# Optimization experiments

Hardware: AMD Instinct MI355X
Metric: run time of the kernel (lower is better)

## Reference

```python
import jax, jax.numpy as jnp
import numpy as np

DIM = 1024

def setup_inputs() -> dict:
    key = jax.random.key(0)
    k1, k2, k3, k4 = jax.random.split(key, 4)
    x = jax.random.normal(k1, (8, 2048, DIM), dtype=jnp.float32)
    # torch Linear weights: y = x @ W.T
    w_qkv = jax.random.normal(k2, (3 * DIM, DIM), dtype=jnp.float32) * (DIM ** -0.5)
    w_proj = jax.random.normal(k3, (DIM, DIM), dtype=jnp.float32) * (DIM ** -0.5)
    b_proj = jax.random.normal(k4, (DIM,), dtype=jnp.float32) * 0.01
    return {"x": x, "w_qkv": w_qkv, "w_proj": w_proj, "b_proj": b_proj}

def reference(x, w_qkv, w_proj, b_proj):
    B, N, C = x.shape
    scale = C ** -0.5
    qkv = jnp.einsum('bnc,dc->bnd', x, w_qkv).reshape(B, N, 3, C)
    q, k, v = qkv[:, :, 0], qkv[:, :, 1], qkv[:, :, 2]  # each [B,N,C]
    attn = jnp.einsum('bnc,bmc->bnm', q, k) * scale      # [B,N,N]
    attn = jax.nn.softmax(attn, axis=-1)
    o = jnp.einsum('bnm,bmc->bnc', attn, v)              # [B,N,C]
    # faithful to torch: (attn@v).transpose(1,2).reshape(B,N,C) permutes data
    o = jnp.swapaxes(o, 1, 2).reshape(B, N, C)
    return jnp.einsum('bnc,dc->bnd', o, w_proj) + b_proj
```

## Files before the change

kernel.cpp:

```cpp
#include <hip/hip_runtime.h>

typedef __bf16 bf16x8_t __attribute__((ext_vector_type(8)));
typedef float f32x4_t __attribute__((ext_vector_type(4)));

#define AS1 __attribute__((address_space(1)))
#define AS3 __attribute__((address_space(3)))

__device__ __forceinline__ unsigned short f2b(float f) {
    unsigned u = __builtin_bit_cast(unsigned, f);
    u += 0x7fffu + ((u >> 16) & 1u);
    return (unsigned short)(u >> 16);
}
__device__ __forceinline__ float b2f(unsigned short s) {
    return __builtin_bit_cast(float, (unsigned)s << 16);
}

__global__ __launch_bounds__(256) void k_f2b(const float* __restrict__ in,
                                             unsigned short* __restrict__ out,
                                             int n4) {
    int i = blockIdx.x * 256 + threadIdx.x;
    if (i >= n4) return;
    float4 v = reinterpret_cast<const float4*>(in)[i];
    ushort4 o;
    o.x = f2b(v.x); o.y = f2b(v.y); o.z = f2b(v.z); o.w = f2b(v.w);
    reinterpret_cast<ushort4*>(out)[i] = o;
}

#define STAGE3(tt, bb) do {                                                    \
    char* dst_ = smem + (bb) * 24576;                                          \
    const size_t kof_ = (size_t)(tt) * 32;                                     \
    __builtin_amdgcn_global_load_lds((const AS1 void*)(pA0 + kof_),            \
        (AS3 void*)(dst_ + wave * 1024), 16, 0, 0);                            \
    __builtin_amdgcn_global_load_lds((const AS1 void*)(pA1 + kof_),            \
        (AS3 void*)(dst_ + 8192 + wave * 1024), 16, 0, 0);                     \
    __builtin_amdgcn_global_load_lds((const AS1 void*)(pB0 + kof_),            \
        (AS3 void*)(dst_ + 16384 + wave * 1024), 16, 0, 0);                    \
} while (0)

__device__ __forceinline__ void gemm_ml_128(
    const unsigned short* __restrict__ A, int lda,
    const unsigned short* __restrict__ B, int ldb,
    int K, char* smem, f32x4_t acc[4][4]) {
    const int tid = threadIdx.x;
    const int wave = tid >> 6, lane = tid & 63;
    const int wm = wave >> 1, wn = wave & 1;
    const int fr = lane & 15, g = lane >> 4;

    const int scolB = ((lane & 3) * 16) ^ (((lane >> 3) & 3) << 4);
    const unsigned short* pA0 = A + (size_t)(wave * 16 + (lane >> 2)) * lda + (scolB >> 1);
    const unsigned short* pA1 = pA0 + (size_t)128 * lda;
    const unsigned short* pB0 = B + (size_t)(wave * 16 + (lane >> 2)) * ldb + (scolB >> 1);

    const int rswz = (g * 16) ^ (((fr >> 1) & 3) << 4);
    int offA[4], offB[4];
#pragma unroll
    for (int mi = 0; mi < 4; ++mi)
        offA[mi] = (wm * 64 + mi * 16 + fr) * 64 + rswz;
#pragma unroll
    for (int ni = 0; ni < 4; ++ni)
        offB[ni] = 16384 + (wn * 64 + ni * 16 + fr) * 64 + rswz;

#pragma unroll
    for (int mi = 0; mi < 4; ++mi)
#pragma unroll
        for (int ni = 0; ni < 4; ++ni)
            acc[mi][ni] = (f32x4_t){0.f, 0.f, 0.f, 0.f};

    const int NT = K >> 5;

    STAGE3(0, 0);
    STAGE3(1, 1);

    int cb = 0;
    for (int t = 0; t < NT; ++t) {
        if (t + 1 < NT) asm volatile("s_waitcnt vmcnt(3)" ::: "memory");
        else            asm volatile("s_waitcnt vmcnt(0)" ::: "memory");
        asm volatile("s_barrier" ::: "memory");
        if (t + 2 < NT) {
            int sb = cb + 2; if (sb >= 3) sb -= 3;
            STAGE3(t + 2, sb);
        }
        const char* rb = smem + cb * 24576;
        bf16x8_t af[4], bfv[4];
#pragma unroll
        for (int mi = 0; mi < 4; ++mi)
            af[mi] = *reinterpret_cast<const bf16x8_t*>(rb + offA[mi]);
#pragma unroll
        for (int ni = 0; ni < 4; ++ni)
            bfv[ni] = *reinterpret_cast<const bf16x8_t*>(rb + offB[ni]);
        __builtin_amdgcn_s_setprio(1);
#pragma unroll
        for (int mi = 0; mi < 4; ++mi)
#pragma unroll
            for (int ni = 0; ni < 4; ++ni)
                acc[mi][ni] = __builtin_amdgcn_mfma_f32_16x16x32_bf16(
                    af[mi], bfv[ni], acc[mi][ni], 0, 0, 0);
        __builtin_amdgcn_s_setprio(0);
        cb = (cb + 1 == 3) ? 0 : cb + 1;
    }
}

#define E128_IDX                                                \
    const int lane = threadIdx.x & 63, wave = threadIdx.x >> 6; \
    const int e_r0 = (wave >> 1) * 64 + (lane >> 4) * 4;        \
    const int e_c0 = (wave & 1) * 64 + (lane & 15);

#define E128_LOOP(...)                                          \
    _Pragma("unroll") for (int mi = 0; mi < 4; ++mi)            \
    _Pragma("unroll") for (int ni = 0; ni < 4; ++ni)            \
    _Pragma("unroll") for (int j = 0; j < 4; ++j) { __VA_ARGS__ }

#define STA(h, i)                                                              \
    __builtin_amdgcn_global_load_lds(                                         \
        (const AS1 void*)(pA + kof + (size_t)((h) * 128 + (i) * 8) * lda),    \
        (AS3 void*)(wb + (h) * 16384 + wave * 2048 + (i) * 1024), 16, 0, 0)
#define STB(h, i)                                                              \
    __builtin_amdgcn_global_load_lds(                                         \
        (const AS1 void*)(pB + kof + (size_t)((h) * 128 + (i) * 8) * ldb),    \
        (AS3 void*)(wb + 32768 + (h) * 16384 + wave * 2048 + (i) * 1024), 16, 0, 0)

#define READ_A(qm)                                                             \
    _Pragma("unroll") for (int mi = 0; mi < 4; ++mi)                           \
        _Pragma("unroll") for (int ks = 0; ks < 2; ++ks)                       \
            af[mi][ks] = *reinterpret_cast<const bf16x8_t*>(rb + offA[qm][mi][ks]);
#define READ_B(qn)                                                             \
    _Pragma("unroll") for (int ni = 0; ni < 2; ++ni)                           \
        _Pragma("unroll") for (int ks = 0; ks < 2; ++ks)                       \
            bf[qn][ni][ks] = *reinterpret_cast<const bf16x8_t*>(rb + offB[qn][ni][ks]);

#define MFMA_QUAD(qm, qn)                                                      \
    __builtin_amdgcn_s_setprio(1);                                             \
    _Pragma("unroll") for (int mi = 0; mi < 4; ++mi)                           \
        _Pragma("unroll") for (int ni = 0; ni < 2; ++ni) {                     \
            acc[qm][qn][mi][ni] = __builtin_amdgcn_mfma_f32_16x16x32_bf16(     \
                af[mi][0], bf[qn][ni][0], acc[qm][qn][mi][ni], 0, 0, 0);       \
            acc[qm][qn][mi][ni] = __builtin_amdgcn_mfma_f32_16x16x32_bf16(     \
                af[mi][1], bf[qn][ni][1], acc[qm][qn][mi][ni], 0, 0, 0);       \
        }                                                                      \
    __builtin_amdgcn_s_setprio(0);

template <bool LAST>
__device__ __forceinline__ void tile_step(
    const char* rb, char* wb, size_t kof,
    const unsigned short* pA, const unsigned short* pB, int lda, int ldb,
    int wave, const int offA[2][4][2], const int offB[2][2][2],
    f32x4_t acc[2][2][4][2]) {
    bf16x8_t af[4][2], bf[2][2][2];
    asm volatile("s_waitcnt vmcnt(2)" ::: "memory");
    asm volatile("s_barrier" ::: "memory");
    if constexpr (!LAST) { STA(0, 0); STA(0, 1); STB(0, 0); STB(0, 1); }
    READ_A(0); READ_B(0); READ_B(1);
    MFMA_QUAD(0, 0);
    MFMA_QUAD(0, 1);
    if constexpr (LAST) asm volatile("s_waitcnt vmcnt(0)" ::: "memory");
    else                asm volatile("s_waitcnt vmcnt(4)" ::: "memory");
    asm volatile("s_barrier" ::: "memory");
    if constexpr (!LAST) { STB(1, 0); STB(1, 1); STA(1, 0); STA(1, 1); }
    READ_A(1);
    MFMA_QUAD(1, 1);
    MFMA_QUAD(1, 0);
}

__device__ __forceinline__ void gemm_ml_256(
    const unsigned short* __restrict__ A, int lda,
    const unsigned short* __restrict__ B, int ldb,
    int K, char* smem, f32x4_t acc[2][2][4][2]) {
    const int tid = threadIdx.x;
    const int wave = tid >> 6, lane = tid & 63;
    const int wsm = (wave >> 2) & 1, wsn = wave & 3;
    const int fr = lane & 15, g = lane >> 4;
    const int srow8 = lane >> 3;
    const int scolB = ((lane & 7) * 16) ^ (srow8 << 4);

    const unsigned short* pA = A + (size_t)(wave * 16 + srow8) * lda + (scolB >> 1);
    const unsigned short* pB = B + (size_t)(wave * 16 + srow8) * ldb + (scolB >> 1);

    int offA[2][4][2], offB[2][2][2];
#pragma unroll
    for (int qm = 0; qm < 2; ++qm)
#pragma unroll
        for (int mi = 0; mi < 4; ++mi)
#pragma unroll
            for (int ks = 0; ks < 2; ++ks)
                offA[qm][mi][ks] = qm * 16384 + (wsm * 64 + mi * 16 + fr) * 128 +
                                   ((ks * 64 + g * 16) ^ ((fr & 7) << 4));
#pragma unroll
    for (int qn = 0; qn < 2; ++qn)
#pragma unroll
        for (int ni = 0; ni < 2; ++ni)
#pragma unroll
            for (int ks = 0; ks < 2; ++ks)
                offB[qn][ni][ks] = 32768 + qn * 16384 + (wsn * 32 + ni * 16 + fr) * 128 +
                                   ((ks * 64 + g * 16) ^ ((fr & 7) << 4));

#pragma unroll
    for (int qm = 0; qm < 2; ++qm)
#pragma unroll
        for (int qn = 0; qn < 2; ++qn)
#pragma unroll
            for (int mi = 0; mi < 4; ++mi)
#pragma unroll
                for (int ni = 0; ni < 2; ++ni)
                    acc[qm][qn][mi][ni] = (f32x4_t){0.f, 0.f, 0.f, 0.f};

    const int NT = K >> 6;

    {
        char* wb = smem;
        const size_t kof = 0;
        STA(0, 0); STA(0, 1);
        STB(0, 0); STB(0, 1);
        STB(1, 0); STB(1, 1);
        STA(1, 0); STA(1, 1);
    }

    for (int t = 0; t < NT - 1; ++t) {
        const char* rb = smem + (size_t)(t & 1) * 65536;
        char* wb = smem + (size_t)((t & 1) ^ 1) * 65536;
        tile_step<false>(rb, wb, (size_t)(t + 1) * 64, pA, pB, lda, ldb,
                         wave, offA, offB, acc);
    }
    {
        const char* rb = smem + (size_t)((NT - 1) & 1) * 65536;
        tile_step<true>(rb, smem, 0, pA, pB, lda, ldb, wave, offA, offB, acc);
    }
}

#define E256_IDX                                                \
    const int lane = threadIdx.x & 63, wave = threadIdx.x >> 6; \
    const int e_r0 = ((wave >> 2) & 1) * 64 + (lane >> 4) * 4;  \
    const int e_c0 = (wave & 3) * 32 + (lane & 15);

#define E256_LOOP(...)                                          \
    _Pragma("unroll") for (int qm = 0; qm < 2; ++qm)            \
    _Pragma("unroll") for (int qn = 0; qn < 2; ++qn)            \
    _Pragma("unroll") for (int mi = 0; mi < 4; ++mi)            \
    _Pragma("unroll") for (int ni = 0; ni < 2; ++ni)            \
    _Pragma("unroll") for (int j = 0; j < 4; ++j) { __VA_ARGS__ }


__global__ __launch_bounds__(512, 4) void k_gemm_qkv_qk(
    const unsigned short* __restrict__ x, const unsigned short* __restrict__ w,
    unsigned short* __restrict__ qk) {
    __shared__ __align__(16) char smem[73728];
    const size_t tm = (size_t)blockIdx.x * 256, tn = (size_t)blockIdx.y * 128;
    f32x4_t acc[4][4];
    gemm_ml_128(x + tm * 1024, 1024, w + tn * 1024, 1024, 1024, smem, acc);
    E128_IDX
    E128_LOOP(
        size_t m = tm + e_r0 + mi * 16 + j;
        size_t z = m >> 11;
        size_t nloc = m & 2047;
        int n = (int)tn + e_c0 + ni * 16;
        unsigned short v = f2b(acc[mi][ni][j]);
        size_t base = z * 4194304 + nloc * 1024;
        if (n < 1024) qk[base + n] = v;
        else          qk[base + 2097152 + (n - 1024)] = v;
    )
}

__global__ __launch_bounds__(512, 2) void k_gemm_vt(
    const unsigned short* __restrict__ wv, const unsigned short* __restrict__ x,
    unsigned short* __restrict__ vt) {
    __shared__ __align__(16) char smem[131072];
    const size_t tm = (size_t)blockIdx.x * 256, tn = (size_t)blockIdx.y * 256;
    f32x4_t acc[2][2][4][2];
    gemm_ml_256(wv + tm * 1024, 1024, x + tn * 1024, 1024, 1024, smem, acc);
    E256_IDX
    E256_LOOP(
        size_t m = tm + qm * 128 + e_r0 + mi * 16 + j;
        size_t n = tn + qn * 128 + e_c0 + ni * 16;
        vt[m * 16384 + n] = f2b(acc[qm][qn][mi][ni][j]);
    )
}

__global__ __launch_bounds__(512, 2) void k_gemm_scores(
    const unsigned short* __restrict__ qk, unsigned short* __restrict__ S, int z0) {
    __shared__ __align__(16) char smem[131072];
    const size_t z = z0 + blockIdx.z;
    const size_t tm = (size_t)blockIdx.x * 256, tn = (size_t)blockIdx.y * 256;
    const unsigned short* qz = qk + z * 4194304;
    const unsigned short* kz = qz + 2097152;
    f32x4_t acc[2][2][4][2];
    gemm_ml_256(qz + tm * 1024, 1024, kz + tn * 1024, 1024, 1024, smem, acc);
    E256_IDX
    unsigned short* Sz = S + (size_t)blockIdx.z * 4194304;
    E256_LOOP(
        size_t m = tm + qm * 128 + e_r0 + mi * 16 + j;
        size_t n = tn + qn * 128 + e_c0 + ni * 16;
        Sz[m * 2048 + n] = f2b(acc[qm][qn][mi][ni][j] * 0.03125f);
    )
}

__global__ __launch_bounds__(256) void k_softmax(const unsigned short* __restrict__ S,
                                                 unsigned short* __restrict__ qk,
                                                 int z0) {
    const size_t r = blockIdx.x;
    const int t = threadIdx.x, wv = t >> 6, ln = t & 63;
    const uint4 u = reinterpret_cast<const uint4*>(S + r * 2048)[t];
    float vals[8];
    vals[0] = b2f((unsigned short)(u.x & 0xffff)); vals[1] = b2f((unsigned short)(u.x >> 16));
    vals[2] = b2f((unsigned short)(u.y & 0xffff)); vals[3] = b2f((unsigned short)(u.y >> 16));
    vals[4] = b2f((unsigned short)(u.z & 0xffff)); vals[5] = b2f((unsigned short)(u.z >> 16));
    vals[6] = b2f((unsigned short)(u.w & 0xffff)); vals[7] = b2f((unsigned short)(u.w >> 16));

    float mx = vals[0];
#pragma unroll
    for (int i = 1; i < 8; ++i) mx = fmaxf(mx, vals[i]);
#pragma unroll
    for (int i = 32; i > 0; i >>= 1) mx = fmaxf(mx, __shfl_xor(mx, i, 64));
    __shared__ float red[8];
    if (ln == 0) red[wv] = mx;
    __syncthreads();
    mx = fmaxf(fmaxf(red[0], red[1]), fmaxf(red[2], red[3]));

    float ex[8], s = 0.f;
#pragma unroll
    for (int i = 0; i < 8; ++i) { ex[i] = __expf(vals[i] - mx); s += ex[i]; }
#pragma unroll
    for (int i = 32; i > 0; i >>= 1) s += __shfl_xor(s, i, 64);
    if (ln == 0) red[4 + wv] = s;
    __syncthreads();
    s = (red[4] + red[5]) + (red[6] + red[7]);
    float inv = 1.0f / s;

    uint4 o;
    o.x = (unsigned)f2b(ex[0] * inv) | ((unsigned)f2b(ex[1] * inv) << 16);
    o.y = (unsigned)f2b(ex[2] * inv) | ((unsigned)f2b(ex[3] * inv) << 16);
    o.z = (unsigned)f2b(ex[4] * inv) | ((unsigned)f2b(ex[5] * inv) << 16);
    o.w = (unsigned)f2b(ex[6] * inv) | ((unsigned)f2b(ex[7] * inv) << 16);

    const size_t zg = z0 + (r >> 11), nloc = r & 2047;
    reinterpret_cast<uint4*>(qk + zg * 4194304 + nloc * 2048)[t] = o;
}

__global__ __launch_bounds__(512, 2) void k_gemm_pv(
    const unsigned short* __restrict__ vt, const unsigned short* __restrict__ qk,
    unsigned short* __restrict__ ob, int z0) {
    __shared__ __align__(16) char smem[131072];
    const size_t z = z0 + blockIdx.z;
    const size_t tm = (size_t)blockIdx.x * 256, tn = (size_t)blockIdx.y * 256;
    const unsigned short* P = qk + z * 4194304;
    f32x4_t acc[2][2][4][2];
    gemm_ml_256(vt + tm * 16384 + z * 2048, 16384,
                P + tn * 2048, 2048, 2048, smem, acc);
    E256_IDX
    unsigned short* oz = ob + z * 2097152;
    E256_LOOP(
        size_t m = tm + qm * 128 + e_r0 + mi * 16 + j;
        size_t n = tn + qn * 128 + e_c0 + ni * 16;
        oz[(2 * m + (n >> 10)) * 1024 + (n & 1023)] = f2b(acc[qm][qn][mi][ni][j]);
    )
}

__global__ __launch_bounds__(512, 2) void k_gemm_proj(
    const unsigned short* __restrict__ o2, const unsigned short* __restrict__ w,
    const float* __restrict__ bias, float* __restrict__ out) {
    __shared__ __align__(16) char smem[131072];
    const size_t tm = (size_t)blockIdx.x * 256, tn = (size_t)blockIdx.y * 256;
    f32x4_t acc[2][2][4][2];
    gemm_ml_256(o2 + tm * 1024, 1024, w + tn * 1024, 1024, 1024, smem, acc);
    E256_IDX
    E256_LOOP(
        size_t m = tm + qm * 128 + e_r0 + mi * 16 + j;
        size_t n = tn + qn * 128 + e_c0 + ni * 16;
        out[m * 1024 + n] = acc[qm][qn][mi][ni][j] + bias[n];
    )
}

extern "C" void kernel_launch(void* const* d_in, const int* in_sizes, int n_in,
                              void* d_out, int out_size, void* d_ws, size_t ws_size,
                              hipStream_t stream) {
    const float* x     = (const float*)d_in[0];
    const float* wqkv  = (const float*)d_in[1];
    const float* wproj = (const float*)d_in[2];
    const float* bproj = (const float*)d_in[3];
    float* out = (float*)d_out;
    char* ws = (char*)d_ws;

    const size_t off_xb    = 0;
    const size_t off_wqkv  = 33554432;
    const size_t off_wproj = 39845888;
    const size_t off_qk    = 41943040;
    const size_t off_vt    = 109051904;
    const size_t off_S     = 142606336;
    int NZ = 0;
    for (int c = 8; c >= 1; c >>= 1)
        if (off_S + (size_t)c * 8388608 <= ws_size) { NZ = c; break; }
    if (NZ == 0) return;

    unsigned short* xb     = (unsigned short*)(ws + off_xb);
    unsigned short* wqkvb  = (unsigned short*)(ws + off_wqkv);
    unsigned short* wprojb = (unsigned short*)(ws + off_wproj);
    unsigned short* qkb    = (unsigned short*)(ws + off_qk);
    unsigned short* vtb    = (unsigned short*)(ws + off_vt);
    unsigned short* Sb     = (unsigned short*)(ws + off_S);
    unsigned short* obuf   = (unsigned short*)(ws + off_xb);

    k_f2b<<<16384, 256, 0, stream>>>(x, xb, 4194304);
    k_f2b<<<3072, 256, 0, stream>>>(wqkv, wqkvb, 786432);
    k_f2b<<<1024, 256, 0, stream>>>(wproj, wprojb, 262144);

    k_gemm_qkv_qk<<<dim3(64, 16), 512, 0, stream>>>(xb, wqkvb, qkb);
    k_gemm_vt<<<dim3(4, 64), 512, 0, stream>>>(wqkvb + (size_t)2048 * 1024, xb, vtb);

    for (int z0 = 0; z0 < 8; z0 += NZ) {
        k_gemm_scores<<<dim3(8, 8, NZ), 512, 0, stream>>>(qkb, Sb, z0);
        k_softmax<<<NZ * 2048, 256, 0, stream>>>(Sb, qkb, z0);
        k_gemm_pv<<<dim3(4, 8, NZ), 512, 0, stream>>>(vtb, qkb, obuf, z0);
    }
    k_gemm_proj<<<dim3(64, 4), 512, 0, stream>>>(obuf, wprojb, bproj, out);
}
```

Baseline: 335.8 us.

## Add finer-grained pipelined GEMM mainloop for scores and PV kernels

Adds a new GEMM mainloop that processes two K tiles per iteration and interleaves per-quadrant LDS reads, global-to-LDS async loads and MFMA quadrants, with barriers between each phase. It is used in the scores and PV GEMMs, while the shared setup code moves into a helper. The aim is to hide global load latency and LDS read latency behind MFMA work more evenly than the old two-phase tile step. It adds many barriers and hand-tuned waitcnt values, which risks synchronisation stalls or subtle ordering hazards. It also assumes an even number of K tiles.

```diff
diff --git a/kernel.cpp b/kernel.cpp
--- a/kernel.cpp
+++ b/kernel.cpp
@@ -138,6 +138,39 @@
                 af[mi][1], bf[qn][ni][1], acc[qm][qn][mi][ni], 0, 0, 0);       \
         }                                                                      \
     __builtin_amdgcn_s_setprio(0);
+
+__device__ __forceinline__ void setup_256(
+    const unsigned short* __restrict__ A, int lda,
+    const unsigned short* __restrict__ B, int ldb,
+    const unsigned short*& pA, const unsigned short*& pB,
+    int offA[2][4][2], int offB[2][2][2]) {
+    const int tid = threadIdx.x;
+    const int wave = tid >> 6, lane = tid & 63;
+    const int wsm = (wave >> 2) & 1, wsn = wave & 3;
+    const int fr = lane & 15, g = lane >> 4;
+    const int srow8 = lane >> 3;
+    const int scolB = ((lane & 7) * 16) ^ (srow8 << 4);
+
+    pA = A + (size_t)(wave * 16 + srow8) * lda + (scolB >> 1);
+    pB = B + (size_t)(wave * 16 + srow8) * ldb + (scolB >> 1);
+
+#pragma unroll
+    for (int qm = 0; qm < 2; ++qm)
+#pragma unroll
+        for (int mi = 0; mi < 4; ++mi)
+#pragma unroll
+            for (int ks = 0; ks < 2; ++ks)
+                offA[qm][mi][ks] = qm * 16384 + (wsm * 64 + mi * 16 + fr) * 128 +
+                                   ((ks * 64 + g * 16) ^ ((fr & 7) << 4));
+#pragma unroll
+    for (int qn = 0; qn < 2; ++qn)
+#pragma unroll
+        for (int ni = 0; ni < 2; ++ni)
+#pragma unroll
+            for (int ks = 0; ks < 2; ++ks)
+                offB[qn][ni][ks] = 32768 + qn * 16384 + (wsn * 32 + ni * 16 + fr) * 128 +
+                                   ((ks * 64 + g * 16) ^ ((fr & 7) << 4));
+}
 
 template <bool LAST>
 __device__ __forceinline__ void tile_step(
@@ -165,33 +198,11 @@
     const unsigned short* __restrict__ A, int lda,
     const unsigned short* __restrict__ B, int ldb,
     int K, char* smem, f32x4_t acc[2][2][4][2]) {
-    const int tid = threadIdx.x;
-    const int wave = tid >> 6, lane = tid & 63;
-    const int wsm = (wave >> 2) & 1, wsn = wave & 3;
-    const int fr = lane & 15, g = lane >> 4;
-    const int srow8 = lane >> 3;
-    const int scolB = ((lane & 7) * 16) ^ (srow8 << 4);
-
-    const unsigned short* pA = A + (size_t)(wave * 16 + srow8) * lda + (scolB >> 1);
-    const unsigned short* pB = B + (size_t)(wave * 16 + srow8) * ldb + (scolB >> 1);
-
+    const int wave = threadIdx.x >> 6;
+    const unsigned short* pA;
+    const unsigned short* pB;
     int offA[2][4][2], offB[2][2][2];
-#pragma unroll
-    for (int qm = 0; qm < 2; ++qm)
-#pragma unroll
-        for (int mi = 0; mi < 4; ++mi)
-#pragma unroll
-            for (int ks = 0; ks < 2; ++ks)
-                offA[qm][mi][ks] = qm * 16384 + (wsm * 64 + mi * 16 + fr) * 128 +
-                                   ((ks * 64 + g * 16) ^ ((fr & 7) << 4));
-#pragma unroll
-    for (int qn = 0; qn < 2; ++qn)
-#pragma unroll
-        for (int ni = 0; ni < 2; ++ni)
-#pragma unroll
-            for (int ks = 0; ks < 2; ++ks)
-                offB[qn][ni][ks] = 32768 + qn * 16384 + (wsn * 32 + ni * 16 + fr) * 128 +
-                                   ((ks * 64 + g * 16) ^ ((fr & 7) << 4));
+    setup_256(A, lda, B, ldb, pA, pB, offA, offB);
 
 #pragma unroll
     for (int qm = 0; qm < 2; ++qm)
@@ -204,7 +215,6 @@
                     acc[qm][qn][mi][ni] = (f32x4_t){0.f, 0.f, 0.f, 0.f};
 
     const int NT = K >> 6;
-
     {
         char* wb = smem;
         const size_t kof = 0;
@@ -213,7 +223,6 @@
         STB(1, 0); STB(1, 1);
         STA(1, 0); STA(1, 1);
     }
-
     for (int t = 0; t < NT - 1; ++t) {
         const char* rb = smem + (size_t)(t & 1) * 65536;
         char* wb = smem + (size_t)((t & 1) ^ 1) * 65536;
@@ -223,6 +232,127 @@
     {
         const char* rb = smem + (size_t)((NT - 1) & 1) * 65536;
         tile_step<true>(rb, smem, 0, pA, pB, lda, ldb, wave, offA, offB, acc);
+    }
+}
+
+#define SCA(d, h, kt) do {                                                     \
+    char* db_ = smem + (d) * 65536 + (h) * 16384 + wave * 2048;                \
+    __builtin_amdgcn_global_load_lds(                                          \
+        (const AS1 void*)(pA + (kt) + (size_t)((h) * 128) * lda),              \
+        (AS3 void*)db_, 16, 0, 0);                                             \
+    __builtin_amdgcn_global_load_lds(                                          \
+        (const AS1 void*)(pA + (kt) + (size_t)((h) * 128 + 8) * lda),          \
+        (AS3 void*)(db_ + 1024), 16, 0, 0);                                    \
+} while (0)
+#define SCB(d, h, kt) do {                                                     \
+    char* db_ = smem + (d) * 65536 + 32768 + (h) * 16384 + wave * 2048;        \
+    __builtin_amdgcn_global_load_lds(                                          \
+        (const AS1 void*)(pB + (kt) + (size_t)((h) * 128) * ldb),              \
+        (AS3 void*)db_, 16, 0, 0);                                             \
+    __builtin_amdgcn_global_load_lds(                                          \
+        (const AS1 void*)(pB + (kt) + (size_t)((h) * 128 + 8) * ldb),          \
+        (AS3 void*)(db_ + 1024), 16, 0, 0);                                    \
+} while (0)
+
+#define C_RA(d, qm)                                                            \
+    _Pragma("unroll") for (int mi = 0; mi < 4; ++mi)                           \
+    _Pragma("unroll") for (int ks = 0; ks < 2; ++ks)                           \
+        af[mi][ks] = *reinterpret_cast<const bf16x8_t*>(                       \
+            smem + (d) * 65536 + offA[qm][mi][ks]);
+#define C_RB(d, qn, B_)                                                        \
+    _Pragma("unroll") for (int ni = 0; ni < 2; ++ni)                           \
+    _Pragma("unroll") for (int ks = 0; ks < 2; ++ks)                           \
+        B_[ni][ks] = *reinterpret_cast<const bf16x8_t*>(                       \
+            smem + (d) * 65536 + offB[qn][ni][ks]);
+
+#define C_MQ(qm, qn, B_)                                                       \
+    __builtin_amdgcn_s_setprio(1);                                             \
+    _Pragma("unroll") for (int mi = 0; mi < 4; ++mi)                           \
+    _Pragma("unroll") for (int ni = 0; ni < 2; ++ni) {                         \
+        acc[qm][qn][mi][ni] = __builtin_amdgcn_mfma_f32_16x16x32_bf16(         \
+            af[mi][0], B_[ni][0], acc[qm][qn][mi][ni], 0, 0, 0);               \
+        acc[qm][qn][mi][ni] = __builtin_amdgcn_mfma_f32_16x16x32_bf16(         \
+            af[mi][1], B_[ni][1], acc[qm][qn][mi][ni], 0, 0, 0);               \
+    }                                                                          \
+    __builtin_amdgcn_s_setprio(0);
+
+#define C_BAR  __builtin_amdgcn_s_barrier()
+#define C_LGK0 do { asm volatile("s_waitcnt lgkmcnt(0)");                      \
+                    __builtin_amdgcn_sched_barrier(0); } while (0)
+
+__device__ __forceinline__ void gemm_ml_256c(
+    const unsigned short* __restrict__ A, int lda,
+    const unsigned short* __restrict__ B, int ldb,
+    int K, char* smem, f32x4_t acc[2][2][4][2]) {
+    const int wave = threadIdx.x >> 6;
+    const unsigned short* pA;
+    const unsigned short* pB;
+    int offA[2][4][2], offB[2][2][2];
+    setup_256(A, lda, B, ldb, pA, pB, offA, offB);
+
+#pragma unroll
+    for (int qm = 0; qm < 2; ++qm)
+#pragma unroll
+        for (int qn = 0; qn < 2; ++qn)
+#pragma unroll
+            for (int mi = 0; mi < 4; ++mi)
+#pragma unroll
+                for (int ni = 0; ni < 2; ++ni)
+                    acc[qm][qn][mi][ni] = (f32x4_t){0.f, 0.f, 0.f, 0.f};
+
+    const int NT = K >> 6, NI = NT >> 1;
+
+    SCA(0, 0, 0); SCB(0, 0, 0); SCB(0, 1, 0); SCA(0, 1, 0);
+    SCA(1, 0, 64); SCB(1, 0, 64); SCB(1, 1, 64);
+    asm volatile("s_waitcnt vmcnt(6)");
+    C_BAR;
+
+    size_t kk = 0;
+    for (int it = 0; it < NI; ++it, kk += 128) {
+        const bool L = (it == NI - 1);
+        const size_t kt1 = kk + 64, kt2 = kk + 128, kt3 = kk + 192;
+        bf16x8_t af[4][2], b0[2][2], b1[2][2];
+        C_RA(0, 0); C_RB(0, 0, b0);
+        SCA(1, 1, kt1);
+        asm volatile("s_waitcnt lgkmcnt(8)");
+        C_BAR; C_LGK0;
+        C_MQ(0, 0, b0);
+        C_BAR;
+        C_RB(0, 1, b1);
+        if (!L) SCA(0, 0, kt2);
+        C_BAR; C_LGK0;
+        C_MQ(0, 1, b1);
+        C_BAR;
+        C_RA(0, 1);
+        if (!L) SCB(0, 0, kt2);
+        C_BAR; C_LGK0;
+        C_MQ(1, 1, b1);
+        C_BAR;
+        if (!L) { SCB(0, 1, kt2); asm volatile("s_waitcnt vmcnt(6)"); }
+        else    { asm volatile("s_waitcnt vmcnt(0)"); }
+        C_BAR;
+        C_MQ(1, 0, b0);
+        C_BAR;
+        C_RA(1, 0); C_RB(1, 0, b0);
+        if (!L) SCA(0, 1, kt2);
+        asm volatile("s_waitcnt lgkmcnt(8)");
+        C_BAR; C_LGK0;
+        C_MQ(0, 0, b0);
+        C_BAR;
+        C_RB(1, 1, b1);
+        if (!L) SCA(1, 0, kt3);
+        C_BAR; C_LGK0;
+        C_MQ(0, 1, b1);
+        C_BAR;
+        C_RA(1, 1);
+        if (!L) SCB(1, 0, kt3);
+        C_BAR; C_LGK0;
+        C_MQ(1, 1, b1);
+        C_BAR;
+        if (!L) { SCB(1, 1, kt3); asm volatile("s_waitcnt vmcnt(6)"); }
+        C_BAR;
+        C_MQ(1, 0, b0);
+        C_BAR;
     }
 }
 
@@ -282,7 +412,7 @@
     const unsigned short* qz = qk + z * 4194304;
     const unsigned short* kz = qz + 2097152;
     f32x4_t acc[2][2][4][2];
-    gemm_ml_256(qz + tm * 1024, 1024, kz + tn * 1024, 1024, 1024, smem, acc);
+    gemm_ml_256c(qz + tm * 1024, 1024, kz + tn * 1024, 1024, 1024, smem, acc);
     E256_IDX
     unsigned short* Sz = S + (size_t)blockIdx.z * 4194304;
     E256_LOOP(
@@ -342,8 +472,8 @@
     const size_t tm = (size_t)blockIdx.x * 256, tn = (size_t)blockIdx.y * 256;
     const unsigned short* P = qk + z * 4194304;
     f32x4_t acc[2][2][4][2];
-    gemm_ml_256(vt + tm * 16384 + z * 2048, 16384,
-                P + tn * 2048, 2048, 2048, smem, acc);
+    gemm_ml_256c(vt + tm * 16384 + z * 2048, 16384,
+                 P + tn * 2048, 2048, 2048, smem, acc);
     E256_IDX
     unsigned short* oz = ob + z * 2097152;
     E256_LOOP(
```

Result: no change. 337.6 us (+0.5%).
